# Optimization experiments

Measured on AMD Instinct MI355X. Metric: run time of the kernel, lower is better.

The kernel has to match this reference:

```python
import jax, jax.numpy as jnp
import numpy as np

L_XYZ = 10  # fourier freqs for position -> 3 + 6*10 = 63 dims
L_DIR = 4   # fourier freqs for direction -> 3 + 6*4 = 27 dims
DIM = 32    # radiance feature dim per depth layer
PPP = 4     # points (depth layers) per pixel
HID = 128   # MLP hidden width
UCH = 64    # UNet hidden channels


def pe(x, L):
    # fourier positional encoding: [x, sin(2^k x), cos(2^k x)]
    f = (2.0 ** jnp.arange(L)).astype(x.dtype)
    xf = x[..., None] * f  # [..., 3, L]
    s = jnp.sin(xf).reshape(x.shape[:-1] + (-1,))
    c = jnp.cos(xf).reshape(x.shape[:-1] + (-1,))
    return jnp.concatenate([x, s, c], axis=-1)


def conv(x, w, b):
    y = jax.lax.conv_general_dilated(x, w, (1, 1), 'SAME',
                                     dimension_numbers=('NCHW', 'OIHW', 'NCHW'))
    return y + b[None, :, None, None]


def setup_inputs() -> dict:
    key = jax.random.key(0)
    ks = jax.random.split(key, 24)
    H = W = 384
    zbufs = jax.random.uniform(ks[0], (H, W, PPP), dtype=jnp.float32)  # depths in [0,1)
    o = jax.random.normal(ks[1], (H, W, 3), dtype=jnp.float32)
    d = jax.random.normal(ks[2], (H, W, 3), dtype=jnp.float32)
    d = d / jnp.linalg.norm(d, axis=-1, keepdims=True)
    cos = jax.random.uniform(ks[3], (H, W, 1), dtype=jnp.float32) * 0.5 + 0.5
    ray = jnp.concatenate([o, d, cos], axis=-1)  # [H,W,7]
    gt = jax.random.uniform(ks[4], (H, W, 3), dtype=jnp.float32)
    mask_gt = jnp.ones((H, W, 1), dtype=jnp.float32)
    xyz_o = jax.random.normal(ks[5], (1024, 3), dtype=jnp.float32)
    in_xyz = 3 + 6 * L_XYZ
    in_dir = 3 + 6 * L_DIR
    in_ch = DIM * PPP
    p = {}
    p['w1'] = jax.random.normal(ks[6], (in_xyz, HID), dtype=jnp.float32) * 0.05
    p['b1'] = jnp.zeros((HID,), dtype=jnp.float32)
    p['w2'] = jax.random.normal(ks[7], (HID, HID), dtype=jnp.float32) * 0.05
    p['b2'] = jnp.zeros((HID,), dtype=jnp.float32)
    p['w3'] = jax.random.normal(ks[8], (HID + in_dir, DIM), dtype=jnp.float32) * 0.05
    p['b3'] = jnp.zeros((DIM,), dtype=jnp.float32)
    p['mpn_w1'] = jax.random.normal(ks[9], (in_ch, in_ch, 3, 3), dtype=jnp.float32) * 0.02
    p['mpn_b1'] = jnp.zeros((in_ch,), dtype=jnp.float32)
    p['mpn_w2'] = jax.random.normal(ks[10], (in_ch, in_ch, 3, 3), dtype=jnp.float32) * 0.02
    p['mpn_b2'] = jnp.zeros((in_ch,), dtype=jnp.float32)
    p['uw1'] = jax.random.normal(ks[11], (UCH, in_ch, 3, 3), dtype=jnp.float32) * 0.02
    p['ub1'] = jnp.zeros((UCH,), dtype=jnp.float32)
    p['uw2'] = jax.random.normal(ks[12], (UCH, UCH, 3, 3), dtype=jnp.float32) * 0.02
    p['ub2'] = jnp.zeros((UCH,), dtype=jnp.float32)
    p['uw3'] = jax.random.normal(ks[13], (3, UCH, 3, 3), dtype=jnp.float32) * 0.02
    p['ub3'] = jnp.zeros((3,), dtype=jnp.float32)
    inp = {'zbufs': zbufs, 'ray': ray, 'gt': gt, 'mask_gt': mask_gt,
           'isTrain': 1, 'xyz_o': xyz_o}
    inp.update(p)
    return inp


def reference(zbufs, ray, gt, mask_gt, isTrain, xyz_o,
              w1, b1, w2, b2, w3, b3,
              mpn_w1, mpn_b1, mpn_w2, mpn_b2,
              uw1, ub1, uw2, ub2, uw3, ub3):
    H, W, P = zbufs.shape
    o = ray[..., :3]
    dirs = ray[..., 3:6]
    cos = ray[..., 6:7]
    thresh = 0.2 if isTrain else 0.0
    # dense equivalent of boolean-mask gather -> MLP -> scatter into zeros
    mask = (zbufs > thresh).astype(zbufs.dtype)  # [H,W,P]
    # xyz_near = o + dirs * zbuf / cos  (xyznear path)
    xyz = o[..., None, :] + dirs[..., None, :] * zbufs[..., None] / cos[..., None]  # [H,W,P,3]
    x = pe(xyz, L_XYZ)                                   # [H,W,P,63]
    h = jax.nn.relu(x @ w1 + b1)                         # [H,W,P,HID]
    h = jax.nn.relu(h @ w2 + b2)
    dpe = pe(dirs, L_DIR)                                # [H,W,27]
    dpe = jnp.broadcast_to(dpe[..., None, :], h.shape[:-1] + (dpe.shape[-1],))
    feat = jnp.concatenate([h, dpe], axis=-1) @ w3 + b3  # [H,W,P,DIM]
    feat = feat * mask[..., None]                        # zeros where pix_mask is False
    # per-layer permute(2,3,0,1) + cat(dim=1) == [1, P*DIM, H, W]
    rdmp = feat.transpose(2, 3, 0, 1).reshape(1, P * DIM, H, W)
    # MPN: predicted per-channel mask
    m = jax.nn.sigmoid(conv(jax.nn.relu(conv(rdmp, mpn_w1, mpn_b1)), mpn_w2, mpn_b2))
    fuse = rdmp * m
    fea_map = jax.nn.sigmoid(fuse[0, :3].transpose(1, 2, 0))  # [H,W,3]
    # UNet refinement to RGB
    u = jax.nn.relu(conv(fuse, uw1, ub1))
    u = jax.nn.relu(conv(u, uw2, ub2))
    img = jax.nn.sigmoid(conv(u, uw3, ub3))[0].transpose(1, 2, 0)  # [H,W,3]
    return img
```

## Files before the change

kernel.cpp:

```cpp
#include <hip/hip_runtime.h>
#include <hip/hip_bf16.h>
#include <math.h>

typedef __attribute__((ext_vector_type(8))) unsigned short ushort8;
typedef __attribute__((ext_vector_type(8))) __bf16 bf16x8;
typedef __attribute__((ext_vector_type(4))) float floatx4;

constexpr int IMGW = 384;
constexpr int NPIX = IMGW * IMGW;

__device__ __forceinline__ unsigned short f2bf(float f) {
  union { float f; unsigned u; } v; v.f = f;
  unsigned u = v.u;
  return (unsigned short)((u + 0x7fffu + ((u >> 16) & 1u)) >> 16);
}
__device__ __forceinline__ float bf2f(unsigned short h) {
  union { unsigned u; float f; } v; v.u = ((unsigned)h) << 16; return v.f;
}
__device__ __forceinline__ unsigned pk2bf(float a, float b) {
  float2 f2; f2.x = a; f2.y = b;
  __hip_bfloat162 h = __float22bfloat162_rn(f2);
  union { __hip_bfloat162 h; unsigned u; } u; u.h = h; return u.u;
}
__device__ __forceinline__ floatx4 mfma16(bf16x8 a, bf16x8 b, floatx4 c) {
  return __builtin_amdgcn_mfma_f32_16x16x32_bf16(a, b, c, 0, 0, 0);
}
__device__ __forceinline__ bf16x8 lds_frag(const unsigned short* p) {
  return *reinterpret_cast<const bf16x8*>(p);
}
__device__ __forceinline__ bf16x8 u4_to_bf(uint4 v) {
  union { uint4 u; bf16x8 b; } c; c.u = v; return c.b;
}

__device__ __forceinline__ void convB_elem(const float* __restrict__ w,
                                           unsigned short* __restrict__ wt,
                                           int i, int CIN, int G, int NT) {
  int j = i & 7, lane = (i >> 3) & 63;
  int rest = i >> 9;
  int nt = rest % NT; int rest2 = rest / NT;
  int g = rest2 % G;  int ks = rest2 / G;
  int q = lane >> 4, m = lane & 15;
  int co = (g * NT + nt) * 16 + m;
  int k = ks * 32 + q * 8 + j;
  int nb = k / CIN, ci = k - nb * CIN;
  wt[i] = f2bf(w[(co * CIN + ci) * 9 + nb]);
}

__global__ __launch_bounds__(256) void prep_all(
    const float* __restrict__ w1, const float* __restrict__ w2, const float* __restrict__ w3,
    const float* __restrict__ mw1, const float* __restrict__ mw2,
    const float* __restrict__ uw1, const float* __restrict__ uw2,
    const float* __restrict__ uw3,
    unsigned short* __restrict__ w1A, unsigned short* __restrict__ w2A,
    unsigned short* __restrict__ w3A,
    unsigned short* __restrict__ cw1, unsigned short* __restrict__ cw2,
    unsigned short* __restrict__ cu1, unsigned short* __restrict__ cu2,
    unsigned short* __restrict__ cu3) {
  int i = blockIdx.x * 256 + threadIdx.x;
  if (i < 29696) {
    if (i < 8192) {
      int j = i & 7, lane = (i >> 3) & 63, t = i >> 9;
      int mt = t >> 1, ks = t & 1;
      int ch_out = mt * 16 + (lane & 15);
      int kp = ks * 32 + (lane >> 4) * 8 + j;
      int chunk = kp >> 3, sl = kp & 7;
      float val;
      if (chunk == 7 && sl >= 4) {
        int c = sl - 4;
        val = (c < 3) ? w1[c * 128 + ch_out] : 0.0f;
      } else {
        const int coordA[8] = {0,0,0,1,1,2,2,2};
        const int octA[8]   = {0,4,8,2,6,0,4,8};
        const int coordB[8] = {0,0,1,1,1,2,2,2};
        const int octB[8]   = {2,6,0,4,8,2,6,0};
        int rc  = (sl < 4) ? coordA[chunk] : coordB[chunk];
        int oct = ((sl < 4) ? octA[chunk] : octB[chunk]) + ((sl >> 1) & 1);
        int korig = ((sl & 1) ? 33 : 3) + rc * 10 + oct;
        val = w1[korig * 128 + ch_out];
      }
      w1A[i] = f2bf(val);
    } else if (i < 24576) {
      int i2 = i - 8192;
      int j = i2 & 7, lane = (i2 >> 3) & 63, t = i2 >> 9;
      int mt = t >> 2, ks = t & 3;
      int ch_out = mt * 16 + (lane & 15);
      int kp = ks * 32 + (lane >> 4) * 8 + j;
      int c_orig = ((kp >> 2) & 7) * 16 + (kp >> 5) * 4 + (kp & 3);
      w2A[i2] = f2bf(w2[c_orig * 128 + ch_out]);
    } else {
      int i3 = i - 24576;
      int j = i3 & 7, lane = (i3 >> 3) & 63, t = i3 >> 9;
      int mt = (t >= 5) ? 1 : 0; int ks = t - mt * 5;
      int q = lane >> 4, m = lane & 15;
      int ch_out = mt * 16 + m;
      float val;
      if (ks < 4) {
        int kp = ks * 32 + q * 8 + j;
        int c_orig = ((kp >> 2) & 7) * 16 + (kp >> 5) * 4 + (kp & 3);
        val = w3[c_orig * 32 + ch_out];
      } else {
        int row = -1;
        if (q == 0) {
          if (j < 3) row = 128 + j;
          else if (j >= 4) {
            int ga = (j - 4) >> 1;
            row = (((j - 4) & 1) == 0 ? 131 : 143) + ga;
          }
        } else {
          int ga = q * 4 - 2 + (j >> 1);
          if (ga < 12) row = ((j & 1) == 0 ? 131 : 143) + ga;
        }
        val = (row >= 0) ? w3[row * 32 + ch_out] : 0.0f;
      }
      w3A[(((mt << 3) + ks) << 9) + (lane << 3) + j] = f2bf(val);
    }
    return;
  }
  i -= 29696;
  if (i < 147456) { convB_elem(mw1, cw1, i, 128, 4, 2); return; }
  i -= 147456;
  if (i < 147456) { convB_elem(mw2, cw2, i, 128, 4, 2); return; }
  i -= 147456;
  if (i < 73728)  { convB_elem(uw1, cu1, i, 128, 4, 1); return; }
  i -= 73728;
  if (i < 36864)  { convB_elem(uw2, cu2, i, 64, 4, 1); return; }
  i -= 36864;
  {
    int j = i & 7, lane = (i >> 3) & 63, ks = i >> 9;
    int q = lane >> 4, m = lane & 15;
    int k = ks * 32 + q * 8 + j;
    int nb = k >> 6, ci = k & 63;
    float val = (m < 3) ? uw3[(m * 64 + ci) * 9 + nb] : 0.0f;
    cu3[i] = f2bf(val);
  }
}

__global__ __launch_bounds__(128, 4) void mlp_kernel(
    const float* __restrict__ zbufs, const float* __restrict__ ray,
    const int* __restrict__ isTrain,
    const float* __restrict__ b1, const float* __restrict__ b2,
    const float* __restrict__ b3,
    const unsigned short* __restrict__ w1A, const unsigned short* __restrict__ w2A,
    const unsigned short* __restrict__ w3A,
    unsigned short* __restrict__ rdmp) {
  __shared__ __align__(16) unsigned short H[64 * 136];

  const int tid = threadIdx.x;
  const int half = tid >> 6;
  const int lane = tid & 63;
  const int q = lane >> 4, m = lane & 15;
  const float thresh = (isTrain[0] != 0) ? 0.2f : 0.0f;

  float fA[2], fB[2];
  int cAi[2], cBi[2];
  #pragma unroll
  for (int ks = 0; ks < 2; ++ks) {
    int ch = ks * 4 + q;
    cAi[ks] = (ch <= 2) ? 0 : ((ch <= 4) ? 1 : 2);
    fA[ks]  = (ch == 0 || ch == 5) ? 1.0f :
              (ch == 1 || ch == 6) ? 16.0f :
              (ch == 2 || ch == 7) ? 256.0f :
              (ch == 3) ? 4.0f : 64.0f;
    cBi[ks] = (ch <= 1) ? 0 : ((ch <= 4) ? 1 : 2);
    fB[ks]  = (ch == 2) ? 1.0f :
              (ch == 0 || ch == 5) ? 4.0f :
              (ch == 3) ? 16.0f :
              (ch == 1 || ch == 6) ? 64.0f : 256.0f;
  }

  bf16x8 bx[4][2];
  bf16x8 dpe0, dpe1;
  float zs[4];
  #pragma unroll
  for (int nt = 0; nt < 4; ++nt) {
    int s = nt * 16 + m;
    int sg = blockIdx.x * 64 + s;
    int pixel = sg >> 2;
    float z = zbufs[sg];
    zs[nt] = z;
    const float* r = ray + (size_t)pixel * 7;
    float t = z / r[6];
    float xv0 = r[0] + r[3] * t, xv1 = r[1] + r[4] * t, xv2 = r[2] + r[5] * t;
    #pragma unroll
    for (int ks = 0; ks < 2; ++ks) {
      float uA = (cAi[ks] == 0) ? xv0 : ((cAi[ks] == 1) ? xv1 : xv2);
      float uB = (cBi[ks] == 0) ? xv0 : ((cBi[ks] == 1) ? xv1 : xv2);
      float sa, ca, sb, cb;
      __sincosf(uA * fA[ks], &sa, &ca);
      __sincosf(uB * fB[ks], &sb, &cb);
      float t2a = sa + sa;
      float sa1 = t2a * ca, ca1 = fmaf(-t2a, sa, 1.0f);
      float t2b = sb + sb;
      float sb1 = t2b * cb, cb1 = fmaf(-t2b, sb, 1.0f);
      if (ks == 1 && q == 3) { sb = xv0; cb = xv1; sb1 = xv2; cb1 = 0.0f; }
      uint4 dv;
      dv.x = pk2bf(sa, ca); dv.y = pk2bf(sa1, ca1);
      dv.z = pk2bf(sb, cb); dv.w = pk2bf(sb1, cb1);
      bx[nt][ks] = u4_to_bf(dv);
    }
    if ((nt >> 1) == half) {
      float dd0 = r[3], dd1 = r[4], dd2 = r[5];
      float ss[4], cc[4];
      #pragma unroll
      for (int ii = 0; ii < 4; ++ii) {
        int a = q * 4 + ii - 2;
        int ac = (a < 0 || a > 11) ? 0 : a;
        int c = ac >> 2;
        float base = (c == 0) ? dd0 : ((c == 1) ? dd1 : dd2);
        float fs = (float)(1 << (ac & 3));
        __sincosf(base * fs, &ss[ii], &cc[ii]);
      }
      uint4 dv;
      if (q == 0) {
        dv.x = pk2bf(dd0, dd1);
        dv.y = pk2bf(dd2, 0.0f);
        dv.z = pk2bf(ss[2], cc[2]);
        dv.w = pk2bf(ss[3], cc[3]);
      } else if (q == 3) {
        dv.x = pk2bf(ss[0], cc[0]);
        dv.y = pk2bf(ss[1], cc[1]);
        dv.z = 0u; dv.w = 0u;
      } else {
        dv.x = pk2bf(ss[0], cc[0]);
        dv.y = pk2bf(ss[1], cc[1]);
        dv.z = pk2bf(ss[2], cc[2]);
        dv.w = pk2bf(ss[3], cc[3]);
      }
      if ((nt & 1) == 0) dpe0 = u4_to_bf(dv); else dpe1 = u4_to_bf(dv);
    }
  }
  float zL[2];
  zL[0] = (half == 0) ? zs[0] : zs[2];
  zL[1] = (half == 0) ? zs[1] : zs[3];

  {
    floatx4 acc[4][4];
    #pragma unroll
    for (int mt = 0; mt < 4; ++mt) {
      float4 bb = *reinterpret_cast<const float4*>(b1 + (half * 4 + mt) * 16 + q * 4);
      #pragma unroll
      for (int nt = 0; nt < 4; ++nt) {
        acc[mt][nt][0] = bb.x; acc[mt][nt][1] = bb.y;
        acc[mt][nt][2] = bb.z; acc[mt][nt][3] = bb.w;
      }
    }
    #pragma unroll
    for (int ks = 0; ks < 2; ++ks) {
      #pragma unroll
      for (int mt = 0; mt < 4; ++mt) {
        int mtg = half * 4 + mt;
        bf16x8 a = *reinterpret_cast<const bf16x8*>(w1A + (((mtg << 1) + ks) << 9) + lane * 8);
        #pragma unroll
        for (int nt = 0; nt < 4; ++nt)
          acc[mt][nt] = mfma16(a, bx[nt][ks], acc[mt][nt]);
      }
    }
    #pragma unroll
    for (int nt = 0; nt < 4; ++nt) {
      uint4* base = reinterpret_cast<uint4*>(&H[(nt * 16 + m) * 136 + q * 32 + half * 16]);
      #pragma unroll
      for (int g = 0; g < 2; ++g) {
        uint4 v;
        v.x = pk2bf(fmaxf(acc[2*g][nt][0], 0.0f),   fmaxf(acc[2*g][nt][1], 0.0f));
        v.y = pk2bf(fmaxf(acc[2*g][nt][2], 0.0f),   fmaxf(acc[2*g][nt][3], 0.0f));
        v.z = pk2bf(fmaxf(acc[2*g+1][nt][0], 0.0f), fmaxf(acc[2*g+1][nt][1], 0.0f));
        v.w = pk2bf(fmaxf(acc[2*g+1][nt][2], 0.0f), fmaxf(acc[2*g+1][nt][3], 0.0f));
        base[g] = v;
      }
    }
  }
  __syncthreads();

  {
    uint4 keep[4][2];
    {
      floatx4 acc[4][4];
      #pragma unroll
      for (int mt = 0; mt < 4; ++mt) {
        float4 bb = *reinterpret_cast<const float4*>(b2 + (half * 4 + mt) * 16 + q * 4);
        #pragma unroll
        for (int nt = 0; nt < 4; ++nt) {
          acc[mt][nt][0] = bb.x; acc[mt][nt][1] = bb.y;
          acc[mt][nt][2] = bb.z; acc[mt][nt][3] = bb.w;
        }
      }
      #pragma unroll 1
      for (int ks = 0; ks < 4; ++ks) {
        bf16x8 bf[4];
        #pragma unroll
        for (int nt = 0; nt < 4; ++nt)
          bf[nt] = lds_frag(H + (nt * 16 + m) * 136 + ks * 32 + q * 8);
        #pragma unroll
        for (int mt = 0; mt < 4; ++mt) {
          int mtg = half * 4 + mt;
          bf16x8 a = *reinterpret_cast<const bf16x8*>(w2A + (((mtg << 2) + ks) << 9) + lane * 8);
          #pragma unroll
          for (int nt = 0; nt < 4; ++nt)
            acc[mt][nt] = mfma16(a, bf[nt], acc[mt][nt]);
        }
      }
      #pragma unroll
      for (int nt = 0; nt < 4; ++nt) {
        #pragma unroll
        for (int g = 0; g < 2; ++g) {
          uint4 v;
          v.x = pk2bf(fmaxf(acc[2*g][nt][0], 0.0f),   fmaxf(acc[2*g][nt][1], 0.0f));
          v.y = pk2bf(fmaxf(acc[2*g][nt][2], 0.0f),   fmaxf(acc[2*g][nt][3], 0.0f));
          v.z = pk2bf(fmaxf(acc[2*g+1][nt][0], 0.0f), fmaxf(acc[2*g+1][nt][1], 0.0f));
          v.w = pk2bf(fmaxf(acc[2*g+1][nt][2], 0.0f), fmaxf(acc[2*g+1][nt][3], 0.0f));
          keep[nt][g] = v;
        }
      }
    }
    __syncthreads();
    #pragma unroll
    for (int nt = 0; nt < 4; ++nt)
      #pragma unroll
      for (int g = 0; g < 2; ++g)
        *reinterpret_cast<uint4*>(&H[(nt * 16 + m) * 136 + q * 32 + half * 16 + g * 8]) = keep[nt][g];
  }
  __syncthreads();

  {
    floatx4 acc[2][2];
    #pragma unroll
    for (int mt = 0; mt < 2; ++mt) {
      float4 bb3 = *reinterpret_cast<const float4*>(b3 + mt * 16 + q * 4);
      #pragma unroll
      for (int nt2 = 0; nt2 < 2; ++nt2) {
        acc[mt][nt2][0] = bb3.x; acc[mt][nt2][1] = bb3.y;
        acc[mt][nt2][2] = bb3.z; acc[mt][nt2][3] = bb3.w;
      }
    }
    #pragma unroll
    for (int mt = 0; mt < 2; ++mt) {
      bf16x8 a = *reinterpret_cast<const bf16x8*>(w3A + (((mt << 3) + 4) << 9) + lane * 8);
      acc[mt][0] = mfma16(a, dpe0, acc[mt][0]);
      acc[mt][1] = mfma16(a, dpe1, acc[mt][1]);
    }
    #pragma unroll 2
    for (int ks = 0; ks < 4; ++ks) {
      bf16x8 bf[2];
      #pragma unroll
      for (int nt2 = 0; nt2 < 2; ++nt2)
        bf[nt2] = lds_frag(H + ((half * 2 + nt2) * 16 + m) * 136 + ks * 32 + q * 8);
      #pragma unroll
      for (int mt = 0; mt < 2; ++mt) {
        bf16x8 a = *reinterpret_cast<const bf16x8*>(w3A + (((mt << 3) + ks) << 9) + lane * 8);
        #pragma unroll
        for (int nt2 = 0; nt2 < 2; ++nt2)
          acc[mt][nt2] = mfma16(a, bf[nt2], acc[mt][nt2]);
      }
    }
    #pragma unroll
    for (int nt2 = 0; nt2 < 2; ++nt2) {
      int s = (half * 2 + nt2) * 16 + m;
      float mk = (zL[nt2] > thresh) ? 1.0f : 0.0f;
      unsigned short* dst = rdmp + (size_t)blockIdx.x * 2048 + s * 32 + q * 4;
      #pragma unroll
      for (int mt = 0; mt < 2; ++mt) {
        uint2 pk;
        pk.x = pk2bf(acc[mt][nt2][0] * mk, acc[mt][nt2][1] * mk);
        pk.y = pk2bf(acc[mt][nt2][2] * mk, acc[mt][nt2][3] * mk);
        *reinterpret_cast<uint2*>(dst + mt * 16) = pk;
      }
    }
  }
}

template<int CIN, int COUT, int MODE, int MINW>
__global__ __launch_bounds__(512, MINW) void conv3x3(
    const unsigned short* __restrict__ in, const unsigned short* __restrict__ wt,
    const float* __restrict__ bias, const unsigned short* __restrict__ rdmp,
    unsigned short* __restrict__ out) {
  constexpr int CP  = CIN + 8;
  constexpr int CH8 = CIN / 8;
  constexpr int KC  = CIN / 32;
  constexpr int NT  = COUT / 64;
  constexpr int GROUPS = KC * 3;
  __shared__ __align__(16) unsigned short lds_in[10 * 18 * CP];

  const int tid = threadIdx.x;
  const int x0 = blockIdx.x * 16, y0 = blockIdx.y * 8;

  for (int i = tid; i < 180 * CH8; i += 512) {
    int pix = i / CH8, part = i - pix * CH8;
    int xx = pix % 18, yy = pix / 18;
    int gx = x0 - 1 + xx, gy = y0 - 1 + yy;
    ushort8 v = {0, 0, 0, 0, 0, 0, 0, 0};
    if (gx >= 0 && gx < IMGW && gy >= 0 && gy < IMGW)
      v = *reinterpret_cast<const ushort8*>(in + ((size_t)(gy * IMGW + gx)) * CIN + part * 8);
    *reinterpret_cast<ushort8*>(&lds_in[pix * CP + part * 8]) = v;
  }
  __syncthreads();

  const int wave = tid >> 6, lane = tid & 63, q = lane >> 4, m = lane & 15;
  const int cw = wave & 3;
  const int rw = wave >> 2;
  floatx4 acc[4][NT] = {};

  auto loadB = [&](int g, bf16x8 (&bb)[3][NT]) {
    int kc = g / 3, dx = g - kc * 3;
    #pragma unroll
    for (int dy = 0; dy < 3; ++dy) {
      int ks = (dy * 3 + dx) * KC + kc;
      #pragma unroll
      for (int nt = 0; nt < NT; ++nt)
        bb[dy][nt] = *reinterpret_cast<const bf16x8*>(
            wt + ((((size_t)ks * 4 + cw) * NT + nt) << 9) + lane * 8);
    }
  };
  auto compute = [&](int g, bf16x8 (&bb)[3][NT]) {
    int kc = g / 3, dx = g - kc * 3;
    bf16x8 a[6];
    #pragma unroll
    for (int rr = 0; rr < 6; ++rr)
      a[rr] = lds_frag(&lds_in[((rw * 4 + rr) * 18 + m + dx) * CP + kc * 32 + q * 8]);
    #pragma unroll
    for (int dy = 0; dy < 3; ++dy)
      #pragma unroll
      for (int nt = 0; nt < NT; ++nt)
        #pragma unroll
        for (int mt = 0; mt < 4; ++mt)
          acc[mt][nt] = mfma16(a[mt + dy], bb[dy][nt], acc[mt][nt]);
  };

  bf16x8 b0[3][NT], b1[3][NT];
  loadB(0, b0);
  #pragma unroll 1
  for (int g = 0; g < GROUPS; g += 2) {
    loadB(g + 1, b1);
    compute(g, b0);
    if (g + 2 < GROUPS) loadB(g + 2, b0);
    compute(g + 1, b1);
  }

  const int co0 = cw * (COUT / 4);
  #pragma unroll
  for (int mt = 0; mt < 4; ++mt) {
    int y = y0 + rw * 4 + mt;
    #pragma unroll
    for (int nt = 0; nt < NT; ++nt) {
      int co = co0 + nt * 16 + m;
      float bb = bias[co];
      #pragma unroll
      for (int r = 0; r < 4; ++r) {
        int pixel = y * IMGW + x0 + q * 4 + r;
        float v = acc[mt][nt][r] + bb;
        if (MODE == 0) {
          v = fmaxf(v, 0.0f);
        } else {
          v = 1.0f / (1.0f + __expf(-v));
          v *= bf2f(rdmp[(size_t)pixel * 128 + co]);
        }
        out[(size_t)pixel * COUT + co] = f2bf(v);
      }
    }
  }
}

__global__ __launch_bounds__(256) void uconv3_kernel(
    const unsigned short* __restrict__ u2, const unsigned short* __restrict__ wt,
    const float* __restrict__ b, float* __restrict__ out) {
  __shared__ __align__(16) unsigned short lds_in[180 * 72];
  const int tid = threadIdx.x;
  const int x0 = blockIdx.x * 16, y0 = blockIdx.y * 8;
  for (int i = tid; i < 180 * 8; i += 256) {
    int pix = i >> 3, part = i & 7;
    int xx = pix % 18, yy = pix / 18;
    int gx = x0 - 1 + xx, gy = y0 - 1 + yy;
    ushort8 v = {0, 0, 0, 0, 0, 0, 0, 0};
    if (gx >= 0 && gx < IMGW && gy >= 0 && gy < IMGW)
      v = *reinterpret_cast<const ushort8*>(u2 + (size_t)(gy * IMGW + gx) * 64 + part * 8);
    *reinterpret_cast<ushort8*>(&lds_in[pix * 72 + part * 8]) = v;
  }
  __syncthreads();
  const int wave = tid >> 6, lane = tid & 63, q = lane >> 4, m = lane & 15;
  floatx4 acc[2] = {};
  #pragma unroll 1
  for (int g = 0; g < 6; ++g) {
    int kc = g / 3, dx = g - kc * 3;
    bf16x8 bb[3];
    #pragma unroll
    for (int dy = 0; dy < 3; ++dy) {
      int ks = (dy * 3 + dx) * 2 + kc;
      bb[dy] = *reinterpret_cast<const bf16x8*>(wt + (ks << 9) + lane * 8);
    }
    bf16x8 a[4];
    #pragma unroll
    for (int rr = 0; rr < 4; ++rr)
      a[rr] = lds_frag(&lds_in[((wave * 2 + rr) * 18 + m + dx) * 72 + kc * 32 + q * 8]);
    #pragma unroll
    for (int dy = 0; dy < 3; ++dy)
      #pragma unroll
      for (int mt = 0; mt < 2; ++mt)
        acc[mt] = mfma16(a[mt + dy], bb[dy], acc[mt]);
  }
  if (m < 3) {
    float bbv = b[m];
    #pragma unroll
    for (int mt = 0; mt < 2; ++mt) {
      int y = y0 + wave * 2 + mt;
      #pragma unroll
      for (int r = 0; r < 4; ++r) {
        int pixel = y * IMGW + x0 + q * 4 + r;
        out[(size_t)pixel * 3 + m] = 1.0f / (1.0f + __expf(-(acc[mt][r] + bbv)));
      }
    }
  }
}

extern "C" void kernel_launch(void* const* d_in, const int* in_sizes, int n_in,
                              void* d_out, int out_size, void* d_ws, size_t ws_size,
                              hipStream_t stream) {
  (void)in_sizes; (void)n_in; (void)out_size; (void)ws_size;
  const float* zbufs = (const float*)d_in[0];
  const float* ray   = (const float*)d_in[1];
  const int* isTrain = (const int*)d_in[4];
  const float* w1 = (const float*)d_in[6];
  const float* b1 = (const float*)d_in[7];
  const float* w2 = (const float*)d_in[8];
  const float* b2 = (const float*)d_in[9];
  const float* w3 = (const float*)d_in[10];
  const float* b3 = (const float*)d_in[11];
  const float* mpn_w1 = (const float*)d_in[12];
  const float* mpn_b1 = (const float*)d_in[13];
  const float* mpn_w2 = (const float*)d_in[14];
  const float* mpn_b2 = (const float*)d_in[15];
  const float* uw1 = (const float*)d_in[16];
  const float* ub1 = (const float*)d_in[17];
  const float* uw2 = (const float*)d_in[18];
  const float* ub2 = (const float*)d_in[19];
  const float* uw3 = (const float*)d_in[20];
  const float* ub3 = (const float*)d_in[21];
  float* out = (float*)d_out;

  unsigned char* ws = (unsigned char*)d_ws;
  size_t off = 0;
  auto alloc = [&](size_t bytes) -> void* {
    void* p = ws + off; off = (off + bytes + 255) & ~(size_t)255; return p;
  };
  unsigned short* w1A  = (unsigned short*)alloc(8192 * 2);
  unsigned short* w2A  = (unsigned short*)alloc(16384 * 2);
  unsigned short* w3A  = (unsigned short*)alloc(8192 * 2);
  unsigned short* cw1  = (unsigned short*)alloc((size_t)128 * 1152 * 2);
  unsigned short* cw2  = (unsigned short*)alloc((size_t)128 * 1152 * 2);
  unsigned short* cu1  = (unsigned short*)alloc((size_t)64 * 1152 * 2);
  unsigned short* cu2  = (unsigned short*)alloc((size_t)64 * 576 * 2);
  unsigned short* cu3  = (unsigned short*)alloc((size_t)9216 * 2);
  unsigned short* rdmp = (unsigned short*)alloc((size_t)NPIX * 128 * 2);
  unsigned short* t1   = (unsigned short*)alloc((size_t)NPIX * 128 * 2);
  unsigned short* fuse = (unsigned short*)alloc((size_t)NPIX * 128 * 2);
  unsigned short* u1 = t1;
  unsigned short* u2 = rdmp;

  prep_all<<<1736, 256, 0, stream>>>(w1, w2, w3, mpn_w1, mpn_w2, uw1, uw2, uw3,
                                     w1A, w2A, w3A, cw1, cw2, cu1, cu2, cu3);
  mlp_kernel<<<NPIX * 4 / 64, 128, 0, stream>>>(zbufs, ray, isTrain, b1, b2, b3,
                                                w1A, w2A, w3A, rdmp);

  dim3 cgrid(IMGW / 16, IMGW / 8);
  conv3x3<128, 128, 0, 4><<<cgrid, 512, 0, stream>>>(rdmp, cw1, mpn_b1, nullptr, t1);
  conv3x3<128, 128, 1, 4><<<cgrid, 512, 0, stream>>>(t1, cw2, mpn_b2, rdmp, fuse);
  conv3x3<128, 64, 0, 4><<<cgrid, 512, 0, stream>>>(fuse, cu1, ub1, nullptr, u1);
  conv3x3<64, 64, 0, 4><<<cgrid, 512, 0, stream>>>(u1, cu2, ub2, nullptr, u2);
  uconv3_kernel<<<cgrid, 256, 0, stream>>>(u2, cu3, ub3, out);
}
```

Baseline: 304.6 us.

## Refactor convs into tile device functions, fully unroll K loop, widen final conv

Turns the conv kernels into device tile functions called from thin wrappers that take a 1D tile index. The manual double-buffered weight prefetch (unroll 1) is replaced by a fully unrolled group loop, leaving load scheduling to the compiler. The final 3-channel conv now uses 512 threads with one row per wave instead of 256 threads with two rows per wave. This likely prepares for a later fused persistent kernel. Full unrolling can raise register pressure under launch_bounds(512,4), and the last conv now does less MFMA work per wave.

```diff
diff --git a/kernel.cpp b/kernel.cpp
--- a/kernel.cpp
+++ b/kernel.cpp
@@ -368,20 +368,19 @@
   }
 }
 
-template<int CIN, int COUT, int MODE, int MINW>
-__global__ __launch_bounds__(512, MINW) void conv3x3(
-    const unsigned short* __restrict__ in, const unsigned short* __restrict__ wt,
-    const float* __restrict__ bias, const unsigned short* __restrict__ rdmp,
-    unsigned short* __restrict__ out) {
+template<int CIN, int COUT, int MODE>
+__device__ __forceinline__ void conv_tile(
+    int tile,
+    const unsigned short* in, const unsigned short* wt,
+    const float* bias, const unsigned short* rdmp,
+    unsigned short* out, unsigned short* lds_in) {
   constexpr int CP  = CIN + 8;
   constexpr int CH8 = CIN / 8;
   constexpr int KC  = CIN / 32;
   constexpr int NT  = COUT / 64;
   constexpr int GROUPS = KC * 3;
-  __shared__ __align__(16) unsigned short lds_in[10 * 18 * CP];
-
   const int tid = threadIdx.x;
-  const int x0 = blockIdx.x * 16, y0 = blockIdx.y * 8;
+  const int x0 = (tile % 24) * 16, y0 = (tile / 24) * 8;
 
   for (int i = tid; i < 180 * CH8; i += 512) {
     int pix = i / CH8, part = i - pix * CH8;
@@ -399,19 +398,18 @@
   const int rw = wave >> 2;
   floatx4 acc[4][NT] = {};
 
-  auto loadB = [&](int g, bf16x8 (&bb)[3][NT]) {
-    int kc = g / 3, dx = g - kc * 3;
+  #pragma unroll
+  for (int g = 0; g < GROUPS; ++g) {
+    const int kc = g / 3, dx = g % 3;
+    bf16x8 b[3][NT];
     #pragma unroll
     for (int dy = 0; dy < 3; ++dy) {
-      int ks = (dy * 3 + dx) * KC + kc;
+      const int ks = (dy * 3 + dx) * KC + kc;
       #pragma unroll
       for (int nt = 0; nt < NT; ++nt)
-        bb[dy][nt] = *reinterpret_cast<const bf16x8*>(
+        b[dy][nt] = *reinterpret_cast<const bf16x8*>(
             wt + ((((size_t)ks * 4 + cw) * NT + nt) << 9) + lane * 8);
     }
-  };
-  auto compute = [&](int g, bf16x8 (&bb)[3][NT]) {
-    int kc = g / 3, dx = g - kc * 3;
     bf16x8 a[6];
     #pragma unroll
     for (int rr = 0; rr < 6; ++rr)
@@ -422,17 +420,7 @@
       for (int nt = 0; nt < NT; ++nt)
         #pragma unroll
         for (int mt = 0; mt < 4; ++mt)
-          acc[mt][nt] = mfma16(a[mt + dy], bb[dy][nt], acc[mt][nt]);
-  };
-
-  bf16x8 b0[3][NT], b1[3][NT];
-  loadB(0, b0);
-  #pragma unroll 1
-  for (int g = 0; g < GROUPS; g += 2) {
-    loadB(g + 1, b1);
-    compute(g, b0);
-    if (g + 2 < GROUPS) loadB(g + 2, b0);
-    compute(g + 1, b1);
+          acc[mt][nt] = mfma16(a[mt + dy], b[dy][nt], acc[mt][nt]);
   }
 
   const int co0 = cw * (COUT / 4);
@@ -459,13 +447,12 @@
   }
 }
 
-__global__ __launch_bounds__(256) void uconv3_kernel(
-    const unsigned short* __restrict__ u2, const unsigned short* __restrict__ wt,
-    const float* __restrict__ b, float* __restrict__ out) {
-  __shared__ __align__(16) unsigned short lds_in[180 * 72];
+__device__ __forceinline__ void uconv_tile(
+    int tile, const unsigned short* u2, const unsigned short* wt,
+    const float* b, float* out, unsigned short* lds_in) {
   const int tid = threadIdx.x;
-  const int x0 = blockIdx.x * 16, y0 = blockIdx.y * 8;
-  for (int i = tid; i < 180 * 8; i += 256) {
+  const int x0 = (tile % 24) * 16, y0 = (tile / 24) * 8;
+  for (int i = tid; i < 180 * 8; i += 512) {
     int pix = i >> 3, part = i & 7;
     int xx = pix % 18, yy = pix / 18;
     int gx = x0 - 1 + xx, gy = y0 - 1 + yy;
@@ -476,38 +463,46 @@
   }
   __syncthreads();
   const int wave = tid >> 6, lane = tid & 63, q = lane >> 4, m = lane & 15;
-  floatx4 acc[2] = {};
-  #pragma unroll 1
+  floatx4 acc = {};
+  #pragma unroll
   for (int g = 0; g < 6; ++g) {
-    int kc = g / 3, dx = g - kc * 3;
+    const int kc = g / 3, dx = g % 3;
     bf16x8 bb[3];
     #pragma unroll
-    for (int dy = 0; dy < 3; ++dy) {
-      int ks = (dy * 3 + dx) * 2 + kc;
-      bb[dy] = *reinterpret_cast<const bf16x8*>(wt + (ks << 9) + lane * 8);
-    }
-    bf16x8 a[4];
-    #pragma unroll
-    for (int rr = 0; rr < 4; ++rr)
-      a[rr] = lds_frag(&lds_in[((wave * 2 + rr) * 18 + m + dx) * 72 + kc * 32 + q * 8]);
-    #pragma unroll
     for (int dy = 0; dy < 3; ++dy)
-      #pragma unroll
-      for (int mt = 0; mt < 2; ++mt)
-        acc[mt] = mfma16(a[mt + dy], bb[dy], acc[mt]);
+      bb[dy] = *reinterpret_cast<const bf16x8*>(wt + ((((dy * 3 + dx) * 2) + kc) << 9) + lane * 8);
+    bf16x8 a[3];
+    #pragma unroll
+    for (int dy = 0; dy < 3; ++dy)
+      a[dy] = lds_frag(&lds_in[((wave + dy) * 18 + m + dx) * 72 + kc * 32 + q * 8]);
+    #pragma unroll
+    for (int dy = 0; dy < 3; ++dy)
+      acc = mfma16(a[dy], bb[dy], acc);
   }
   if (m < 3) {
     float bbv = b[m];
-    #pragma unroll
-    for (int mt = 0; mt < 2; ++mt) {
-      int y = y0 + wave * 2 + mt;
-      #pragma unroll
-      for (int r = 0; r < 4; ++r) {
-        int pixel = y * IMGW + x0 + q * 4 + r;
-        out[(size_t)pixel * 3 + m] = 1.0f / (1.0f + __expf(-(acc[mt][r] + bbv)));
-      }
-    }
-  }
+    int y = y0 + wave;
+    #pragma unroll
+    for (int r = 0; r < 4; ++r) {
+      int pixel = y * IMGW + x0 + q * 4 + r;
+      out[(size_t)pixel * 3 + m] = 1.0f / (1.0f + __expf(-(acc[r] + bbv)));
+    }
+  }
+}
+
+template<int CIN, int COUT, int MODE>
+__global__ __launch_bounds__(512, 4) void conv_wrap(
+    const unsigned short* __restrict__ in, const unsigned short* __restrict__ wt,
+    const float* __restrict__ bias, const unsigned short* __restrict__ rdmp,
+    unsigned short* __restrict__ out) {
+  __shared__ __align__(16) unsigned short lds[10 * 18 * (CIN + 8)];
+  conv_tile<CIN, COUT, MODE>(blockIdx.x, in, wt, bias, rdmp, out, lds);
+}
+__global__ __launch_bounds__(512, 4) void uconv_wrap(
+    const unsigned short* __restrict__ u2, const unsigned short* __restrict__ wt,
+    const float* __restrict__ b, float* __restrict__ out) {
+  __shared__ __align__(16) unsigned short lds[180 * 72];
+  uconv_tile(blockIdx.x, u2, wt, b, out, lds);
 }
 
 extern "C" void kernel_launch(void* const* d_in, const int* in_sizes, int n_in,
@@ -559,10 +554,9 @@
   mlp_kernel<<<NPIX * 4 / 64, 128, 0, stream>>>(zbufs, ray, isTrain, b1, b2, b3,
                                                 w1A, w2A, w3A, rdmp);
 
-  dim3 cgrid(IMGW / 16, IMGW / 8);
-  conv3x3<128, 128, 0, 4><<<cgrid, 512, 0, stream>>>(rdmp, cw1, mpn_b1, nullptr, t1);
-  conv3x3<128, 128, 1, 4><<<cgrid, 512, 0, stream>>>(t1, cw2, mpn_b2, rdmp, fuse);
-  conv3x3<128, 64, 0, 4><<<cgrid, 512, 0, stream>>>(fuse, cu1, ub1, nullptr, u1);
-  conv3x3<64, 64, 0, 4><<<cgrid, 512, 0, stream>>>(u1, cu2, ub2, nullptr, u2);
-  uconv3_kernel<<<cgrid, 256, 0, stream>>>(u2, cu3, ub3, out);
-}
+  conv_wrap<128, 128, 0><<<1152, 512, 0, stream>>>(rdmp, cw1, mpn_b1, nullptr, t1);
+  conv_wrap<128, 128, 1><<<1152, 512, 0, stream>>>(t1, cw2, mpn_b2, rdmp, fuse);
+  conv_wrap<128, 64, 0><<<1152, 512, 0, stream>>>(fuse, cu1, ub1, nullptr, u1);
+  conv_wrap<64, 64, 0><<<1152, 512, 0, stream>>>(u1, cu2, ub2, nullptr, u2);
+  uconv_wrap<<<1152, 512, 0, stream>>>(u2, cu3, ub3, out);
+}
```

After: 333.2 us. +9.4%, slower.
